# Kernel tuning notes

Hardware: AMD Instinct MI355X
Metric: run time of the kernel (lower is better)

## Reference

```python
import jax, jax.numpy as jnp
import numpy as np

T, B, E, H = 2048, 2, 1024, 16
D = E // H  # head_dim = 64

def setup_inputs() -> dict:
    key = jax.random.key(0)
    ks = jax.random.split(key, 9)
    s = 1.0 / np.sqrt(E)
    return {
        "query": jax.random.normal(ks[0], (T, B, E), dtype=jnp.float32),
        "Wq": jax.random.normal(ks[1], (E, E), dtype=jnp.float32) * s,
        "bq": jax.random.normal(ks[2], (E,), dtype=jnp.float32) * 0.02,
        "Wk": jax.random.normal(ks[3], (E, E), dtype=jnp.float32) * s,
        "bk": jax.random.normal(ks[4], (E,), dtype=jnp.float32) * 0.02,
        "Wv": jax.random.normal(ks[5], (E, E), dtype=jnp.float32) * s,
        "bv": jax.random.normal(ks[6], (E,), dtype=jnp.float32) * 0.02,
        "Wo": jax.random.normal(ks[7], (E, E), dtype=jnp.float32) * s,
        "bo": jax.random.normal(ks[8], (E,), dtype=jnp.float32) * 0.02,
    }

def reference(query, Wq, bq, Wk, bk, Wv, bv, Wo, bo):
    # query: [T, B, E] (fairseq Time x Batch x Channel layout)
    t, b, e = query.shape
    scaling = D ** -0.5
    q = (query @ Wq.T + bq) * scaling          # [T,B,E], scaled like fairseq
    k = query @ Wk.T + bk                      # self-attention: k,v from query
    v = query @ Wv.T + bv
    # split heads: [T,B,H,D]
    q = q.reshape(t, b, H, D)
    k = k.reshape(t, b, H, D)
    v = v.reshape(t, b, H, D)
    # attn weights: [B,H,T(tgt),S(src)]
    scores = jnp.einsum("tbhd,sbhd->bhts", q, k)
    probs = jax.nn.softmax(scores, axis=-1)
    # attend: [T,B,H,D] -> [T,B,E]
    ctx = jnp.einsum("bhts,sbhd->tbhd", probs, v).reshape(t, b, e)
    return ctx @ Wo.T + bo                     # [T,B,E]
```

## Files before the change

kernel.cpp:

```cpp
#include <hip/hip_runtime.h>
#include <hip/hip_bf16.h>
#include <math.h>

#define TT 2048
#define BB 2
#define EE 1024
#define HH 16
#define DD 64
#define RR (TT*BB)

typedef __bf16 bf16x8 __attribute__((ext_vector_type(8)));
typedef float  floatx4 __attribute__((ext_vector_type(4)));

__device__ __forceinline__ unsigned short f2b(float f) {
    union { float f; unsigned u; } x{f};
    return (unsigned short)((x.u + 0x7FFFu + ((x.u >> 16) & 1u)) >> 16);
}

__device__ __forceinline__ float exp2_fast(float x) {
    return __builtin_amdgcn_exp2f(x);
}

typedef const __attribute__((address_space(1))) unsigned int as1_u32;
typedef __attribute__((address_space(3))) unsigned int as3_u32;
__device__ __forceinline__ void gload16(const void* g, void* l) {
    __builtin_amdgcn_global_load_lds((as1_u32*)g, (as3_u32*)l, 16, 0, 0);
}

#define SCALE_Q 0.18033688011112042f

__device__ __forceinline__ int swz(int r) {
    return (r & 7) ^ (((r >> 3) & 3) << 1);
}

__global__ __launch_bounds__(256)
void pack_bf16(const float* __restrict__ x,  const float* __restrict__ wq,
               const float* __restrict__ wk, const float* __restrict__ wv,
               const float* __restrict__ wo, unsigned short* __restrict__ dst)
{
    const size_t e0 = ((size_t)blockIdx.x * 256 + threadIdx.x) * 8;
    const float* src;
    if (e0 < (size_t)4 * 1024 * 1024) {
        src = x + e0;
    } else {
        const int seg = (int)((e0 >> 20) - 4);
        const float* wsrc[4] = {wq, wk, wv, wo};
        src = wsrc[seg] + (e0 & ((1u << 20) - 1));
    }
    const float4 a = *(const float4*)src;
    const float4 b = *(const float4*)(src + 4);
    union { unsigned short u[8]; uint4 v; } p;
    p.u[0] = f2b(a.x); p.u[1] = f2b(a.y); p.u[2] = f2b(a.z); p.u[3] = f2b(a.w);
    p.u[4] = f2b(b.x); p.u[5] = f2b(b.y); p.u[6] = f2b(b.z); p.u[7] = f2b(b.w);
    *(uint4*)&dst[e0] = p.v;
}

template<int MODE>
__global__ __launch_bounds__(256)
void gemm_mfma(const unsigned short* __restrict__ A,
               const unsigned short* __restrict__ Bw,
               const float* __restrict__ b0, const float* __restrict__ b1,
               const float* __restrict__ b2,
               void* __restrict__ out0, void* __restrict__ out1,
               void* __restrict__ out2)
{
    constexpr int BM = (MODE == 0) ? 128 : 64;
    constexpr int BN = (MODE == 0) ? 128 : 64;
    constexpr int MT = BM / 32;
    constexpr int NT = BN / 32;
    constexpr int RA = BM / 64;
    constexpr int RB = BN / 64;
    constexpr int SMEM = (MODE == 0) ? 34816 : 8192;
    __shared__ __align__(16) unsigned char smem[SMEM];
    unsigned short* ldsA = (unsigned short*)smem;
    unsigned short* ldsB = (unsigned short*)(smem + BM * 64);

    const int tid  = threadIdx.x;
    const int w    = tid >> 6;
    const int lane = tid & 63;
    const int quad = lane >> 4;
    const int l15  = lane & 15;
    const int wm   = w & 1;
    const int wn   = w >> 1;
    const int i0   = blockIdx.x * BM;
    const int j0   = blockIdx.y * BN;

    const unsigned short* ga[RA];
    const unsigned short* gb[RB];
    #pragma unroll
    for (int r = 0; r < RA; ++r) {
        const int slot = r * 256 + tid;
        const int row  = slot >> 2;
        const int gc   = (slot & 3) ^ ((row >> 1) & 3);
        ga[r] = A + (size_t)(i0 + row) * EE + gc * 8;
    }
    #pragma unroll
    for (int r = 0; r < RB; ++r) {
        const int slot = r * 256 + tid;
        const int row  = slot >> 2;
        const int gc   = (slot & 3) ^ ((row >> 1) & 3);
        gb[r] = Bw + (size_t)(j0 + row) * EE + gc * 8;
    }

    floatx4 acc[MT][NT];
    #pragma unroll
    for (int mt = 0; mt < MT; ++mt)
        #pragma unroll
        for (int nt = 0; nt < NT; ++nt)
            acc[mt][nt] = (floatx4){0.f, 0.f, 0.f, 0.f};

    for (int kk = 0; kk < EE; kk += 32) {
        __syncthreads();
        #pragma unroll
        for (int r = 0; r < RA; ++r)
            gload16(ga[r] + kk, ldsA + (r * 256 + w * 64) * 8);
        #pragma unroll
        for (int r = 0; r < RB; ++r)
            gload16(gb[r] + kk, ldsB + (r * 256 + w * 64) * 8);
        __syncthreads();

        bf16x8 af[MT], bfr[NT];
        #pragma unroll
        for (int mt = 0; mt < MT; ++mt) {
            const int row = wm * (BM / 2) + mt * 16 + l15;
            af[mt] = __builtin_bit_cast(bf16x8,
                *(const uint4*)&ldsA[(row * 4 + (quad ^ ((row >> 1) & 3))) * 8]);
        }
        #pragma unroll
        for (int nt = 0; nt < NT; ++nt) {
            const int col = wn * (BN / 2) + nt * 16 + l15;
            bfr[nt] = __builtin_bit_cast(bf16x8,
                *(const uint4*)&ldsB[(col * 4 + (quad ^ ((col >> 1) & 3))) * 8]);
        }
        #pragma unroll
        for (int mt = 0; mt < MT; ++mt)
            #pragma unroll
            for (int nt = 0; nt < NT; ++nt)
                acc[mt][nt] = __builtin_amdgcn_mfma_f32_16x16x32_bf16(
                    af[mt], bfr[nt], acc[mt][nt], 0, 0, 0);
    }

    if (MODE == 1) {
        float* dst = (float*)out0;
        #pragma unroll
        for (int nt = 0; nt < NT; ++nt) {
            const int j = j0 + wn * (BN / 2) + nt * 16 + l15;
            const float bb = b0[j];
            #pragma unroll
            for (int mt = 0; mt < MT; ++mt) {
                const int i = i0 + wm * (BM / 2) + mt * 16 + quad * 4;
                #pragma unroll
                for (int r2 = 0; r2 < 4; ++r2)
                    dst[(size_t)(i + r2) * EE + j] = acc[mt][nt][r2] + bb;
            }
        }
    } else {
        const int which = j0 >> 10;
        const float scale = (which == 0) ? SCALE_Q : 1.0f;
        const float* bias = (which == 0) ? b0 : (which == 1) ? b1 : b2;
        if (which < 2) {
            unsigned short* dst = (unsigned short*)(which == 0 ? out0 : out1);
            #pragma unroll
            for (int nt = 0; nt < NT; ++nt) {
                const int j = (j0 & 1023) + wn * 64 + nt * 16 + l15;
                const int h = j >> 6, d = j & 63;
                const float bb = bias[j];
                #pragma unroll
                for (int mt = 0; mt < MT; ++mt) {
                    const int i = i0 + wm * 64 + mt * 16 + quad * 4;
                    #pragma unroll
                    for (int r2 = 0; r2 < 4; ++r2) {
                        const int ii = i + r2;
                        const int t = ii >> 1, b = ii & 1;
                        dst[((size_t)(b * HH + h) * TT + t) * DD + d] =
                            f2b((acc[mt][nt][r2] + bb) * scale);
                    }
                }
            }
        } else {
            __syncthreads();
            unsigned short* tr = (unsigned short*)smem + (size_t)w * 64 * 68;
            #pragma unroll
            for (int nt = 0; nt < NT; ++nt) {
                const int jl = nt * 16 + l15;
                const float bb = bias[(j0 & 1023) + wn * 64 + jl];
                #pragma unroll
                for (int mt = 0; mt < MT; ++mt) {
                    const int il0 = mt * 16 + quad * 4;
                    ushort4 h4;
                    h4.x = f2b(acc[mt][nt][0] + bb);
                    h4.y = f2b(acc[mt][nt][1] + bb);
                    h4.z = f2b(acc[mt][nt][2] + bb);
                    h4.w = f2b(acc[mt][nt][3] + bb);
                    *(ushort4*)&tr[jl * 68 + il0] = h4;
                }
            }
            __syncthreads();
            const int jg = (j0 & 1023) + wn * 64 + lane;
            const int h = jg >> 6, d = jg & 63;
            const int tb = (i0 + wm * 64) >> 1;
            const unsigned short* rp = tr + (size_t)lane * 68;
            unsigned short* dstV = (unsigned short*)out2;
            #pragma unroll
            for (int g = 0; g < 4; ++g) {
                union { unsigned short u[8]; uint4 v; } pe, po;
                #pragma unroll
                for (int k = 0; k < 8; ++k) {
                    pe.u[k] = rp[(g * 8 + k) * 2];
                    po.u[k] = rp[(g * 8 + k) * 2 + 1];
                }
                *(uint4*)&dstV[((size_t)(0 * HH + h) * DD + d) * TT + tb + g * 8] = pe.v;
                *(uint4*)&dstV[((size_t)(1 * HH + h) * DD + d) * TT + tb + g * 8] = po.v;
            }
        }
    }
}

__global__ __launch_bounds__(256, 4)
void attn_mfma(const unsigned short* __restrict__ Q,
               const unsigned short* __restrict__ K,
               const unsigned short* __restrict__ Vt,
               unsigned short* __restrict__ ctx)
{
    __shared__ __align__(16) unsigned short ksm[64 * 64];
    __shared__ __align__(16) unsigned short vtm[64 * 64];

    const int tid  = threadIdx.x;
    const int w    = tid >> 6;
    const int lane = tid & 63;
    const int quad = lane >> 4;
    const int l15  = lane & 15;
    const int bh   = blockIdx.x;
    const int tt   = blockIdx.y;

    const unsigned short* Qh = Q  + (size_t)bh * TT * DD;
    const unsigned short* Kh = K  + (size_t)bh * TT * DD;
    const unsigned short* Vh = Vt + (size_t)bh * DD * TT;

    const int q0w = tt * 128 + w * 32;

    bf16x8 qf[2][2];
    #pragma unroll
    for (int qn = 0; qn < 2; ++qn)
        #pragma unroll
        for (int kd = 0; kd < 2; ++kd)
            qf[qn][kd] = __builtin_bit_cast(bf16x8,
                *(const uint4*)&Qh[(size_t)(q0w + qn * 16 + l15) * DD + kd * 32 + quad * 8]);

    const unsigned short* kg[2];
    const unsigned short* vg[2];
    #pragma unroll
    for (int r = 0; r < 2; ++r) {
        const int slot = r * 256 + tid;
        const int row  = slot >> 3;
        const int gc   = (slot & 7) ^ swz(row);
        kg[r] = Kh + (size_t)row * DD + gc * 8;
        vg[r] = Vh + (size_t)row * TT + gc * 8;
    }

    int ofsKA[4][2], ofsVB[4][2];
    #pragma unroll
    for (int mt = 0; mt < 4; ++mt) {
        const int row = ((mt >> 1) << 5) + ((l15 >> 2) << 3) + ((mt & 1) << 2) + (l15 & 3);
        #pragma unroll
        for (int kd = 0; kd < 2; ++kd)
            ofsKA[mt][kd] = row * 64 + (((kd * 4 + quad) ^ swz(row)) << 3);
    }
    #pragma unroll
    for (int dn = 0; dn < 4; ++dn) {
        const int row = dn * 16 + l15;
        #pragma unroll
        for (int ks = 0; ks < 2; ++ks)
            ofsVB[dn][ks] = row * 64 + (((ks * 4 + quad) ^ swz(row)) << 3);
    }

    floatx4 cacc[4][2];
    #pragma unroll
    for (int dn = 0; dn < 4; ++dn)
        #pragma unroll
        for (int qn = 0; qn < 2; ++qn)
            cacc[dn][qn] = (floatx4){0.f, 0.f, 0.f, 0.f};
    float rs[2] = {0.f, 0.f};

    for (int st = 0; st < TT / 64; ++st) {
        __syncthreads();
        gload16(kg[0] + (size_t)st * 64 * DD, ksm + (size_t)(0 * 256 + w * 64) * 8);
        gload16(kg[1] + (size_t)st * 64 * DD, ksm + (size_t)(1 * 256 + w * 64) * 8);
        gload16(vg[0] + (size_t)st * 64,      vtm + (size_t)(0 * 256 + w * 64) * 8);
        gload16(vg[1] + (size_t)st * 64,      vtm + (size_t)(1 * 256 + w * 64) * 8);
        __syncthreads();

        uint2 pk[4][2];
        #pragma unroll
        for (int mt = 0; mt < 4; ++mt) {
            const bf16x8 ka0 = __builtin_bit_cast(bf16x8, *(const uint4*)&ksm[ofsKA[mt][0]]);
            const bf16x8 ka1 = __builtin_bit_cast(bf16x8, *(const uint4*)&ksm[ofsKA[mt][1]]);
            #pragma unroll
            for (int qn = 0; qn < 2; ++qn) {
                floatx4 s = (floatx4){0.f, 0.f, 0.f, 0.f};
                s = __builtin_amdgcn_mfma_f32_16x16x32_bf16(ka0, qf[qn][0], s, 0, 0, 0);
                s = __builtin_amdgcn_mfma_f32_16x16x32_bf16(ka1, qf[qn][1], s, 0, 0, 0);
                const float p0 = exp2_fast(s[0]);
                const float p1 = exp2_fast(s[1]);
                const float p2 = exp2_fast(s[2]);
                const float p3 = exp2_fast(s[3]);
                rs[qn] += (p0 + p1) + (p2 + p3);
                union { __hip_bfloat162 h2[2]; uint2 u; } c;
                c.h2[0] = __float22bfloat162_rn(make_float2(p0, p1));
                c.h2[1] = __float22bfloat162_rn(make_float2(p2, p3));
                pk[mt][qn] = c.u;
            }
        }

        bf16x8 pa[2][2];
        #pragma unroll
        for (int qn = 0; qn < 2; ++qn) {
            union { uint2 d[2]; uint4 v; } a0, a1;
            a0.d[0] = pk[0][qn]; a0.d[1] = pk[1][qn];
            a1.d[0] = pk[2][qn]; a1.d[1] = pk[3][qn];
            pa[qn][0] = __builtin_bit_cast(bf16x8, a0.v);
            pa[qn][1] = __builtin_bit_cast(bf16x8, a1.v);
        }

        #pragma unroll
        for (int dn = 0; dn < 4; ++dn) {
            const bf16x8 vb0 = __builtin_bit_cast(bf16x8, *(const uint4*)&vtm[ofsVB[dn][0]]);
            const bf16x8 vb1 = __builtin_bit_cast(bf16x8, *(const uint4*)&vtm[ofsVB[dn][1]]);
            #pragma unroll
            for (int qn = 0; qn < 2; ++qn) {
                cacc[dn][qn] = __builtin_amdgcn_mfma_f32_16x16x32_bf16(pa[qn][0], vb0, cacc[dn][qn], 0, 0, 0);
                cacc[dn][qn] = __builtin_amdgcn_mfma_f32_16x16x32_bf16(pa[qn][1], vb1, cacc[dn][qn], 0, 0, 0);
            }
        }
    }

    const int b = bh / HH, hh = bh % HH;
    float linv[2];
    #pragma unroll
    for (int qn = 0; qn < 2; ++qn) {
        float t = rs[qn];
        t += __shfl_xor(t, 16);
        t += __shfl_xor(t, 32);
        linv[qn] = 1.0f / t;
    }
    #pragma unroll
    for (int qn = 0; qn < 2; ++qn) {
        float lj[4];
        #pragma unroll
        for (int j = 0; j < 4; ++j)
            lj[j] = __shfl(linv[qn], quad * 4 + j);
        #pragma unroll
        for (int dn = 0; dn < 4; ++dn) {
            const int e = hh * 64 + dn * 16 + l15;
            #pragma unroll
            for (int j = 0; j < 4; ++j) {
                const int t = q0w + qn * 16 + quad * 4 + j;
                ctx[(size_t)(t * BB + b) * EE + e] = f2b(cacc[dn][qn][j] * lj[j]);
            }
        }
    }
}

extern "C" void kernel_launch(void* const* d_in, const int* in_sizes, int n_in,
                              void* d_out, int out_size, void* d_ws, size_t ws_size,
                              hipStream_t stream)
{
    const float* x  = (const float*)d_in[0];
    const float* Wq = (const float*)d_in[1];
    const float* bq = (const float*)d_in[2];
    const float* Wk = (const float*)d_in[3];
    const float* bk = (const float*)d_in[4];
    const float* Wv = (const float*)d_in[5];
    const float* bv = (const float*)d_in[6];
    const float* Wo = (const float*)d_in[7];
    const float* bo = (const float*)d_in[8];
    float* out = (float*)d_out;

    const size_t M1 = 1024 * 1024;
    unsigned short* base = (unsigned short*)d_ws;
    unsigned short* xb   = base;
    unsigned short* wqkv = base + 4 * M1;
    unsigned short* wob  = base + 7 * M1;
    unsigned short* qb   = base + 8 * M1;
    unsigned short* kb   = base + 12 * M1;
    unsigned short* vtb  = base + 16 * M1;
    unsigned short* cb   = base + 20 * M1;

    dim3 blk(256);

    pack_bf16<<<dim3(4096), blk, 0, stream>>>(x, Wq, Wk, Wv, Wo, base);

    gemm_mfma<0><<<dim3(RR / 128, 3072 / 128), blk, 0, stream>>>(
        xb, wqkv, bq, bk, bv, qb, kb, vtb);

    attn_mfma<<<dim3(BB * HH, TT / 128), blk, 0, stream>>>(qb, kb, vtb, cb);

    gemm_mfma<1><<<dim3(RR / 64, EE / 64), blk, 0, stream>>>(
        cb, wob, bo, nullptr, nullptr, out, nullptr, nullptr);
}
```

Baseline: 197.7 us.

## Split attention over key halves with combine pass and deepen GEMM K-tiles

The attention kernel now splits the key range into two halves via a third grid dimension. Each half writes unnormalized bf16 partial context and per-row sums, and a new combine kernel adds them and normalizes. This doubles the number of attention blocks to fill more compute units, and it loads two 64-key tiles per barrier to halve synchronization. The GEMMs use a 64-wide K step with a new swizzle, and the output projection moves to 128-row tiles. The cost is an extra kernel launch and extra memory traffic for the partial buffers, plus added rounding from storing partials in bf16.

```diff
diff --git a/kernel.cpp b/kernel.cpp
--- a/kernel.cpp
+++ b/kernel.cpp
@@ -16,6 +16,12 @@
     union { float f; unsigned u; } x{f};
     return (unsigned short)((x.u + 0x7FFFu + ((x.u >> 16) & 1u)) >> 16);
 }
+__device__ __forceinline__ float b2f_lo(unsigned u) {
+    union { unsigned u; float f; } x{u << 16}; return x.f;
+}
+__device__ __forceinline__ float b2f_hi(unsigned u) {
+    union { unsigned u; float f; } x{u & 0xffff0000u}; return x.f;
+}
 
 __device__ __forceinline__ float exp2_fast(float x) {
     return __builtin_amdgcn_exp2f(x);
@@ -36,23 +42,29 @@
 __global__ __launch_bounds__(256)
 void pack_bf16(const float* __restrict__ x,  const float* __restrict__ wq,
                const float* __restrict__ wk, const float* __restrict__ wv,
-               const float* __restrict__ wo, unsigned short* __restrict__ dst)
+               const float* __restrict__ wo, unsigned short* __restrict__ base,
+               unsigned short* __restrict__ wob)
 {
+    const size_t M4 = (size_t)4 << 20, M7 = (size_t)7 << 20;
     const size_t e0 = ((size_t)blockIdx.x * 256 + threadIdx.x) * 8;
     const float* src;
-    if (e0 < (size_t)4 * 1024 * 1024) {
-        src = x + e0;
+    unsigned short* dst;
+    if (e0 < M4) {
+        src = x + e0; dst = base + e0;
+    } else if (e0 < M7) {
+        const int seg = (int)((e0 >> 20) - 4);
+        const float* wsrc[3] = {wq, wk, wv};
+        src = wsrc[seg] + (e0 & ((1u << 20) - 1));
+        dst = base + e0;
     } else {
-        const int seg = (int)((e0 >> 20) - 4);
-        const float* wsrc[4] = {wq, wk, wv, wo};
-        src = wsrc[seg] + (e0 & ((1u << 20) - 1));
+        src = wo + (e0 - M7); dst = wob + (e0 - M7);
     }
     const float4 a = *(const float4*)src;
     const float4 b = *(const float4*)(src + 4);
     union { unsigned short u[8]; uint4 v; } p;
     p.u[0] = f2b(a.x); p.u[1] = f2b(a.y); p.u[2] = f2b(a.z); p.u[3] = f2b(a.w);
     p.u[4] = f2b(b.x); p.u[5] = f2b(b.y); p.u[6] = f2b(b.z); p.u[7] = f2b(b.w);
-    *(uint4*)&dst[e0] = p.v;
+    *(uint4*)dst = p.v;
 }
 
 template<int MODE>
@@ -64,16 +76,16 @@
                void* __restrict__ out0, void* __restrict__ out1,
                void* __restrict__ out2)
 {
-    constexpr int BM = (MODE == 0) ? 128 : 64;
+    constexpr int BM = 128;
     constexpr int BN = (MODE == 0) ? 128 : 64;
-    constexpr int MT = BM / 32;
-    constexpr int NT = BN / 32;
-    constexpr int RA = BM / 64;
-    constexpr int RB = BN / 64;
-    constexpr int SMEM = (MODE == 0) ? 34816 : 8192;
+    constexpr int MT = 4;
+    constexpr int NT = (MODE == 0) ? 4 : 2;
+    constexpr int RA = BM / 32;
+    constexpr int RB = BN / 32;
+    constexpr int SMEM = (MODE == 0) ? 34816 : 24576;
     __shared__ __align__(16) unsigned char smem[SMEM];
     unsigned short* ldsA = (unsigned short*)smem;
-    unsigned short* ldsB = (unsigned short*)(smem + BM * 64);
+    unsigned short* ldsB = (unsigned short*)(smem + BM * 128);
 
     const int tid  = threadIdx.x;
     const int w    = tid >> 6;
@@ -90,16 +102,32 @@
     #pragma unroll
     for (int r = 0; r < RA; ++r) {
         const int slot = r * 256 + tid;
-        const int row  = slot >> 2;
-        const int gc   = (slot & 3) ^ ((row >> 1) & 3);
+        const int row  = slot >> 3;
+        const int gc   = (slot & 7) ^ swz(row);
         ga[r] = A + (size_t)(i0 + row) * EE + gc * 8;
     }
     #pragma unroll
     for (int r = 0; r < RB; ++r) {
         const int slot = r * 256 + tid;
-        const int row  = slot >> 2;
-        const int gc   = (slot & 3) ^ ((row >> 1) & 3);
+        const int row  = slot >> 3;
+        const int gc   = (slot & 7) ^ swz(row);
         gb[r] = Bw + (size_t)(j0 + row) * EE + gc * 8;
+    }
+
+    int ofsA[2][MT], ofsB[2][NT];
+    #pragma unroll
+    for (int mt = 0; mt < MT; ++mt) {
+        const int row = wm * 64 + mt * 16 + l15;
+        #pragma unroll
+        for (int ks = 0; ks < 2; ++ks)
+            ofsA[ks][mt] = row * 64 + (((ks * 4 + quad) ^ swz(row)) << 3);
+    }
+    #pragma unroll
+    for (int nt = 0; nt < NT; ++nt) {
+        const int col = wn * (BN / 2) + nt * 16 + l15;
+        #pragma unroll
+        for (int ks = 0; ks < 2; ++ks)
+            ofsB[ks][nt] = col * 64 + (((ks * 4 + quad) ^ swz(col)) << 3);
     }
 
     floatx4 acc[MT][NT];
@@ -109,7 +137,7 @@
         for (int nt = 0; nt < NT; ++nt)
             acc[mt][nt] = (floatx4){0.f, 0.f, 0.f, 0.f};
 
-    for (int kk = 0; kk < EE; kk += 32) {
+    for (int kk = 0; kk < EE; kk += 64) {
         __syncthreads();
         #pragma unroll
         for (int r = 0; r < RA; ++r)
@@ -119,36 +147,33 @@
             gload16(gb[r] + kk, ldsB + (r * 256 + w * 64) * 8);
         __syncthreads();
 
-        bf16x8 af[MT], bfr[NT];
-        #pragma unroll
-        for (int mt = 0; mt < MT; ++mt) {
-            const int row = wm * (BM / 2) + mt * 16 + l15;
-            af[mt] = __builtin_bit_cast(bf16x8,
-                *(const uint4*)&ldsA[(row * 4 + (quad ^ ((row >> 1) & 3))) * 8]);
+        #pragma unroll
+        for (int ks = 0; ks < 2; ++ks) {
+            bf16x8 af[MT], bfr[NT];
+            #pragma unroll
+            for (int mt = 0; mt < MT; ++mt)
+                af[mt] = __builtin_bit_cast(bf16x8, *(const uint4*)&ldsA[ofsA[ks][mt]]);
+            #pragma unroll
+            for (int nt = 0; nt < NT; ++nt)
+                bfr[nt] = __builtin_bit_cast(bf16x8, *(const uint4*)&ldsB[ofsB[ks][nt]]);
+            #pragma unroll
+            for (int mt = 0; mt < MT; ++mt)
+                #pragma unroll
+                for (int nt = 0; nt < NT; ++nt)
+                    acc[mt][nt] = __builtin_amdgcn_mfma_f32_16x16x32_bf16(
+                        af[mt], bfr[nt], acc[mt][nt], 0, 0, 0);
         }
-        #pragma unroll
-        for (int nt = 0; nt < NT; ++nt) {
-            const int col = wn * (BN / 2) + nt * 16 + l15;
-            bfr[nt] = __builtin_bit_cast(bf16x8,
-                *(const uint4*)&ldsB[(col * 4 + (quad ^ ((col >> 1) & 3))) * 8]);
-        }
-        #pragma unroll
-        for (int mt = 0; mt < MT; ++mt)
-            #pragma unroll
-            for (int nt = 0; nt < NT; ++nt)
-                acc[mt][nt] = __builtin_amdgcn_mfma_f32_16x16x32_bf16(
-                    af[mt], bfr[nt], acc[mt][nt], 0, 0, 0);
     }
 
     if (MODE == 1) {
         float* dst = (float*)out0;
         #pragma unroll
         for (int nt = 0; nt < NT; ++nt) {
-            const int j = j0 + wn * (BN / 2) + nt * 16 + l15;
+            const int j = j0 + wn * 32 + nt * 16 + l15;
             const float bb = b0[j];
             #pragma unroll
             for (int mt = 0; mt < MT; ++mt) {
-                const int i = i0 + wm * (BM / 2) + mt * 16 + quad * 4;
+                const int i = i0 + wm * 64 + mt * 16 + quad * 4;
                 #pragma unroll
                 for (int r2 = 0; r2 < 4; ++r2)
                     dst[(size_t)(i + r2) * EE + j] = acc[mt][nt][r2] + bb;
@@ -216,14 +241,15 @@
     }
 }
 
-__global__ __launch_bounds__(256, 4)
+__global__ __launch_bounds__(256)
 void attn_mfma(const unsigned short* __restrict__ Q,
                const unsigned short* __restrict__ K,
                const unsigned short* __restrict__ Vt,
-               unsigned short* __restrict__ ctx)
+               unsigned short* __restrict__ cpart,
+               float* __restrict__ lsumbuf)
 {
-    __shared__ __align__(16) unsigned short ksm[64 * 64];
-    __shared__ __align__(16) unsigned short vtm[64 * 64];
+    __shared__ __align__(16) unsigned short ksm[2][64 * 64];
+    __shared__ __align__(16) unsigned short vtm[2][64 * 64];
 
     const int tid  = threadIdx.x;
     const int w    = tid >> 6;
@@ -232,12 +258,14 @@
     const int l15  = lane & 15;
     const int bh   = blockIdx.x;
     const int tt   = blockIdx.y;
+    const int half = blockIdx.z;
 
     const unsigned short* Qh = Q  + (size_t)bh * TT * DD;
     const unsigned short* Kh = K  + (size_t)bh * TT * DD;
     const unsigned short* Vh = Vt + (size_t)bh * DD * TT;
 
-    const int q0w = tt * 128 + w * 32;
+    const int q0w  = tt * 128 + w * 32;
+    const int key0 = half * 1024;
 
     bf16x8 qf[2][2];
     #pragma unroll
@@ -247,15 +275,21 @@
             qf[qn][kd] = __builtin_bit_cast(bf16x8,
                 *(const uint4*)&Qh[(size_t)(q0w + qn * 16 + l15) * DD + kd * 32 + quad * 8]);
 
-    const unsigned short* kg[2];
-    const unsigned short* vg[2];
-    #pragma unroll
-    for (int r = 0; r < 2; ++r) {
+    const unsigned short* kg[4];
+    #pragma unroll
+    for (int r = 0; r < 4; ++r) {
         const int slot = r * 256 + tid;
         const int row  = slot >> 3;
         const int gc   = (slot & 7) ^ swz(row);
-        kg[r] = Kh + (size_t)row * DD + gc * 8;
-        vg[r] = Vh + (size_t)row * TT + gc * 8;
+        kg[r] = Kh + (size_t)(key0 + row) * DD + gc * 8;
+    }
+    const unsigned short* vg[4];
+    #pragma unroll
+    for (int r = 0; r < 4; ++r) {
+        const int s512 = (r & 1) * 256 + tid;
+        const int rowd = s512 >> 3;
+        const int gc   = (s512 & 7) ^ swz(rowd);
+        vg[r] = Vh + (size_t)rowd * TT + key0 + (r >> 1) * 64 + gc * 8;
     }
 
     int ofsKA[4][2], ofsVB[4][2];
@@ -282,83 +316,119 @@
             cacc[dn][qn] = (floatx4){0.f, 0.f, 0.f, 0.f};
     float rs[2] = {0.f, 0.f};
 
-    for (int st = 0; st < TT / 64; ++st) {
+    for (int big = 0; big < 8; ++big) {
+        const size_t ko = (size_t)big * 128;
         __syncthreads();
-        gload16(kg[0] + (size_t)st * 64 * DD, ksm + (size_t)(0 * 256 + w * 64) * 8);
-        gload16(kg[1] + (size_t)st * 64 * DD, ksm + (size_t)(1 * 256 + w * 64) * 8);
-        gload16(vg[0] + (size_t)st * 64,      vtm + (size_t)(0 * 256 + w * 64) * 8);
-        gload16(vg[1] + (size_t)st * 64,      vtm + (size_t)(1 * 256 + w * 64) * 8);
+        gload16(kg[0] + ko * DD, &ksm[0][(size_t)(0 * 256 + w * 64) * 8]);
+        gload16(kg[1] + ko * DD, &ksm[0][(size_t)(1 * 256 + w * 64) * 8]);
+        gload16(kg[2] + ko * DD, &ksm[1][(size_t)(0 * 256 + w * 64) * 8]);
+        gload16(kg[3] + ko * DD, &ksm[1][(size_t)(1 * 256 + w * 64) * 8]);
+        gload16(vg[0] + ko,      &vtm[0][(size_t)(0 * 256 + w * 64) * 8]);
+        gload16(vg[1] + ko,      &vtm[0][(size_t)(1 * 256 + w * 64) * 8]);
+        gload16(vg[2] + ko,      &vtm[1][(size_t)(0 * 256 + w * 64) * 8]);
+        gload16(vg[3] + ko,      &vtm[1][(size_t)(1 * 256 + w * 64) * 8]);
         __syncthreads();
 
-        uint2 pk[4][2];
-        #pragma unroll
-        for (int mt = 0; mt < 4; ++mt) {
-            const bf16x8 ka0 = __builtin_bit_cast(bf16x8, *(const uint4*)&ksm[ofsKA[mt][0]]);
-            const bf16x8 ka1 = __builtin_bit_cast(bf16x8, *(const uint4*)&ksm[ofsKA[mt][1]]);
+        #pragma unroll
+        for (int sub = 0; sub < 2; ++sub) {
+            uint2 pk[4][2];
+            #pragma unroll
+            for (int mt = 0; mt < 4; ++mt) {
+                const bf16x8 ka0 = __builtin_bit_cast(bf16x8, *(const uint4*)&ksm[sub][ofsKA[mt][0]]);
+                const bf16x8 ka1 = __builtin_bit_cast(bf16x8, *(const uint4*)&ksm[sub][ofsKA[mt][1]]);
+                #pragma unroll
+                for (int qn = 0; qn < 2; ++qn) {
+                    floatx4 s = (floatx4){0.f, 0.f, 0.f, 0.f};
+                    s = __builtin_amdgcn_mfma_f32_16x16x32_bf16(ka0, qf[qn][0], s, 0, 0, 0);
+                    s = __builtin_amdgcn_mfma_f32_16x16x32_bf16(ka1, qf[qn][1], s, 0, 0, 0);
+                    const float p0 = exp2_fast(s[0]);
+                    const float p1 = exp2_fast(s[1]);
+                    const float p2 = exp2_fast(s[2]);
+                    const float p3 = exp2_fast(s[3]);
+                    rs[qn] += (p0 + p1) + (p2 + p3);
+                    union { __hip_bfloat162 h2[2]; uint2 u; } c;
+                    c.h2[0] = __float22bfloat162_rn(make_float2(p0, p1));
+                    c.h2[1] = __float22bfloat162_rn(make_float2(p2, p3));
+                    pk[mt][qn] = c.u;
+                }
+            }
+            bf16x8 pa[2][2];
             #pragma unroll
             for (int qn = 0; qn < 2; ++qn) {
-                floatx4 s = (floatx4){0.f, 0.f, 0.f, 0.f};
-                s = __builtin_amdgcn_mfma_f32_16x16x32_bf16(ka0, qf[qn][0], s, 0, 0, 0);
-                s = __builtin_amdgcn_mfma_f32_16x16x32_bf16(ka1, qf[qn][1], s, 0, 0, 0);
-                const float p0 = exp2_fast(s[0]);
-                const float p1 = exp2_fast(s[1]);
-                const float p2 = exp2_fast(s[2]);
-                const float p3 = exp2_fast(s[3]);
-                rs[qn] += (p0 + p1) + (p2 + p3);
-                union { __hip_bfloat162 h2[2]; uint2 u; } c;
-                c.h2[0] = __float22bfloat162_rn(make_float2(p0, p1));
-                c.h2[1] = __float22bfloat162_rn(make_float2(p2, p3));
-                pk[mt][qn] = c.u;
+                union { uint2 d[2]; uint4 v; } a0, a1;
+                a0.d[0] = pk[0][qn]; a0.d[1] = pk[1][qn];
+                a1.d[0] = pk[2][qn]; a1.d[1] = pk[3][qn];
+                pa[qn][0] = __builtin_bit_cast(bf16x8, a0.v);
+                pa[qn][1] = __builtin_bit_cast(bf16x8, a1.v);
+            }
+            #pragma unroll
+            for (int dn = 0; dn < 4; ++dn) {
+                const bf16x8 vb0 = __builtin_bit_cast(bf16x8, *(const uint4*)&vtm[sub][ofsVB[dn][0]]);
+                const bf16x8 vb1 = __builtin_bit_cast(bf16x8, *(const uint4*)&vtm[sub][ofsVB[dn][1]]);
+                #pragma unroll
+                for (int qn = 0; qn < 2; ++qn) {
+                    cacc[dn][qn] = __builtin_amdgcn_mfma_f32_16x16x32_bf16(pa[qn][0], vb0, cacc[dn][qn], 0, 0, 0);
+                    cacc[dn][qn] = __builtin_amdgcn_mfma_f32_16x16x32_bf16(pa[qn][1], vb1, cacc[dn][qn], 0, 0, 0);
+                }
             }
         }
-
-        bf16x8 pa[2][2];
-        #pragma unroll
-        for (int qn = 0; qn < 2; ++qn) {
-            union { uint2 d[2]; uint4 v; } a0, a1;
-            a0.d[0] = pk[0][qn]; a0.d[1] = pk[1][qn];
-            a1.d[0] = pk[2][qn]; a1.d[1] = pk[3][qn];
-            pa[qn][0] = __builtin_bit_cast(bf16x8, a0.v);
-            pa[qn][1] = __builtin_bit_cast(bf16x8, a1.v);
-        }
-
-        #pragma unroll
-        for (int dn = 0; dn < 4; ++dn) {
-            const bf16x8 vb0 = __builtin_bit_cast(bf16x8, *(const uint4*)&vtm[ofsVB[dn][0]]);
-            const bf16x8 vb1 = __builtin_bit_cast(bf16x8, *(const uint4*)&vtm[ofsVB[dn][1]]);
-            #pragma unroll
-            for (int qn = 0; qn < 2; ++qn) {
-                cacc[dn][qn] = __builtin_amdgcn_mfma_f32_16x16x32_bf16(pa[qn][0], vb0, cacc[dn][qn], 0, 0, 0);
-                cacc[dn][qn] = __builtin_amdgcn_mfma_f32_16x16x32_bf16(pa[qn][1], vb1, cacc[dn][qn], 0, 0, 0);
-            }
-        }
     }
 
     const int b = bh / HH, hh = bh % HH;
-    float linv[2];
+    float rsw[2];
     #pragma unroll
     for (int qn = 0; qn < 2; ++qn) {
         float t = rs[qn];
         t += __shfl_xor(t, 16);
         t += __shfl_xor(t, 32);
-        linv[qn] = 1.0f / t;
-    }
+        rsw[qn] = t;
+    }
+    unsigned short* cp = cpart + (size_t)half * RR * EE;
     #pragma unroll
     for (int qn = 0; qn < 2; ++qn) {
-        float lj[4];
-        #pragma unroll
-        for (int j = 0; j < 4; ++j)
-            lj[j] = __shfl(linv[qn], quad * 4 + j);
         #pragma unroll
         for (int dn = 0; dn < 4; ++dn) {
             const int e = hh * 64 + dn * 16 + l15;
             #pragma unroll
             for (int j = 0; j < 4; ++j) {
                 const int t = q0w + qn * 16 + quad * 4 + j;
-                ctx[(size_t)(t * BB + b) * EE + e] = f2b(cacc[dn][qn][j] * lj[j]);
+                cp[(size_t)(t * BB + b) * EE + e] = f2b(cacc[dn][qn][j]);
             }
         }
     }
+    if (quad == 0) {
+        lsumbuf[(half * BB * HH + bh) * TT + q0w + 0 * 16 + l15] = rsw[0];
+        lsumbuf[(half * BB * HH + bh) * TT + q0w + 1 * 16 + l15] = rsw[1];
+    }
+}
+
+__global__ __launch_bounds__(256)
+void combine(const unsigned short* __restrict__ cpart,
+             const float* __restrict__ lsumbuf,
+             unsigned short* __restrict__ cb)
+{
+    const int gid = blockIdx.x * 256 + threadIdx.x;
+    const int e0 = (gid & 127) * 8;
+    const int r  = gid >> 7;
+    const int t = r >> 1, b = r & 1;
+    const int h = e0 >> 6;
+    const int bh = b * HH + h;
+    const float inv = 1.0f /
+        (lsumbuf[bh * TT + t] + lsumbuf[(BB * HH + bh) * TT + t]);
+    const uint4 c0 = *(const uint4*)&cpart[(size_t)r * EE + e0];
+    const uint4 c1 = *(const uint4*)&cpart[(size_t)RR * EE + (size_t)r * EE + e0];
+    const unsigned u0[4] = {c0.x, c0.y, c0.z, c0.w};
+    const unsigned u1[4] = {c1.x, c1.y, c1.z, c1.w};
+    union { unsigned u[4]; uint4 v; } o;
+    #pragma unroll
+    for (int k = 0; k < 4; ++k) {
+        const float lo = (b2f_lo(u0[k]) + b2f_lo(u1[k])) * inv;
+        const float hi = (b2f_hi(u0[k]) + b2f_hi(u1[k])) * inv;
+        union { __hip_bfloat162 h2; unsigned u; } pk;
+        pk.h2 = __float22bfloat162_rn(make_float2(lo, hi));
+        o.u[k] = pk.u;
+    }
+    *(uint4*)&cb[(size_t)r * EE + e0] = o.v;
 }
 
 extern "C" void kernel_launch(void* const* d_in, const int* in_sizes, int n_in,
@@ -376,25 +446,29 @@
     const float* bo = (const float*)d_in[8];
     float* out = (float*)d_out;
 
-    const size_t M1 = 1024 * 1024;
-    unsigned short* base = (unsigned short*)d_ws;
-    unsigned short* xb   = base;
-    unsigned short* wqkv = base + 4 * M1;
-    unsigned short* wob  = base + 7 * M1;
-    unsigned short* qb   = base + 8 * M1;
-    unsigned short* kb   = base + 12 * M1;
-    unsigned short* vtb  = base + 16 * M1;
-    unsigned short* cb   = base + 20 * M1;
+    const size_t M1 = (size_t)1 << 20;
+    unsigned short* base  = (unsigned short*)d_ws;
+    unsigned short* xb    = base;
+    unsigned short* wqkv  = base + 4 * M1;
+    unsigned short* cpart = base;
+    unsigned short* qb    = base + 8 * M1;
+    unsigned short* kb    = base + 12 * M1;
+    unsigned short* vtb   = base + 16 * M1;
+    unsigned short* cb    = base + 20 * M1;
+    unsigned short* wob   = base + 24 * M1;
+    float*          lsum  = (float*)(base + 25 * M1);
 
     dim3 blk(256);
 
-    pack_bf16<<<dim3(4096), blk, 0, stream>>>(x, Wq, Wk, Wv, Wo, base);
+    pack_bf16<<<dim3(4096), blk, 0, stream>>>(x, Wq, Wk, Wv, Wo, base, wob);
 
     gemm_mfma<0><<<dim3(RR / 128, 3072 / 128), blk, 0, stream>>>(
         xb, wqkv, bq, bk, bv, qb, kb, vtb);
 
-    attn_mfma<<<dim3(BB * HH, TT / 128), blk, 0, stream>>>(qb, kb, vtb, cb);
-
-    gemm_mfma<1><<<dim3(RR / 64, EE / 64), blk, 0, stream>>>(
+    attn_mfma<<<dim3(BB * HH, TT / 128, 2), blk, 0, stream>>>(qb, kb, vtb, cpart, lsum);
+
+    combine<<<dim3(RR * EE / 8 / 256), blk, 0, stream>>>(cpart, lsum, cb);
+
+    gemm_mfma<1><<<dim3(RR / 128, EE / 64), blk, 0, stream>>>(
         cb, wob, bo, nullptr, nullptr, out, nullptr, nullptr);
 }
```

Result: no change. 196.8 us (-0.5%).
